# Kernel tuning notes

Measured on AMD Instinct MI355X. Metric: run time of the kernel, lower is better.

## Reference

```python
import jax, jax.numpy as jnp
import numpy as np

T, B, D, H = 512, 128, 256, 256
SIGMA = 0.01


def setup_inputs() -> dict:
    key = jax.random.key(0)
    ks = jax.random.split(key, 5)
    inputs = jax.random.normal(ks[0], (T, B, D), dtype=jnp.float32)
    W_xh_f = jax.random.normal(ks[1], (D, H), dtype=jnp.float32) * SIGMA
    W_hh_f = jax.random.normal(ks[2], (H, H), dtype=jnp.float32) * SIGMA
    b_h_f = jnp.zeros((H,), dtype=jnp.float32)
    W_xh_b = jax.random.normal(ks[3], (D, H), dtype=jnp.float32) * SIGMA
    W_hh_b = jax.random.normal(ks[4], (H, H), dtype=jnp.float32) * SIGMA
    b_h_b = jnp.zeros((H,), dtype=jnp.float32)
    return {"inputs": inputs, "W_xh_f": W_xh_f, "W_hh_f": W_hh_f, "b_h_f": b_h_f,
            "W_xh_b": W_xh_b, "W_hh_b": W_hh_b, "b_h_b": b_h_b}


def _rnn(inputs, W_xh, W_hh, b_h):
    # inputs: [T, B, D]; returns outputs [T, B, H], final state [B, H]
    h0 = jnp.zeros((inputs.shape[1], W_hh.shape[0]), dtype=inputs.dtype)
    # Precompute input projections for all steps (one big GEMM).
    xW = jnp.einsum('tbd,dh->tbh', inputs, W_xh) + b_h

    def step(h, xw_t):
        h = jnp.tanh(xw_t + h @ W_hh)
        return h, h

    hT, outs = jax.lax.scan(step, h0, xW)
    return outs, hT


def reference(inputs, W_xh_f, W_hh_f, b_h_f, W_xh_b, W_hh_b, b_h_b):
    f_outs, f_H = _rnn(inputs, W_xh_f, W_hh_f, b_h_f)          # forward direction
    b_outs, b_H = _rnn(inputs[::-1], W_xh_b, W_hh_b, b_h_b)    # backward direction
    # align backward outputs with original time order and concat on feature dim
    outputs = jnp.concatenate([f_outs, b_outs[::-1]], axis=-1)  # [T, B, 2H]
    return outputs, f_H, b_H
```

## Files before the change

kernel.cpp:

```cpp
#include <hip/hip_runtime.h>
#include <hip/hip_bf16.h>
#include <stdint.h>


typedef short sh8   __attribute__((ext_vector_type(8)));
typedef float f32x4 __attribute__((ext_vector_type(4)));

#define TT 512
#define BB 128
#define HH 256
#define LDH 264

__device__ __forceinline__ unsigned short f2bf(float x) {
    union { float f; unsigned u; } v; v.f = x;
    unsigned r = v.u + 0x7FFFu + ((v.u >> 16) & 1u);
    return (unsigned short)(r >> 16);
}
__device__ __forceinline__ unsigned pk2bf(float lo, float hi) {
    union { __hip_bfloat162 b; unsigned u; } c;
    c.b = __float22bfloat162_rn(make_float2(lo, hi));
    return c.u;
}
__device__ __forceinline__ float tanh5(float x) {
    float e = __builtin_amdgcn_exp2f(x * 2.8853900817779268f);
    return __builtin_fmaf(-2.0f, __builtin_amdgcn_rcpf(e + 1.0f), 1.0f);
}
__device__ __forceinline__ void bar_lds() {
    asm volatile("s_waitcnt lgkmcnt(0)\n\ts_barrier" ::: "memory");
}
__device__ __forceinline__ sh8 pack8(float4 a, float4 b) {
    union { sh8 s; unsigned u[4]; } c;
    c.u[0] = pk2bf(a.x, a.y); c.u[1] = pk2bf(a.z, a.w);
    c.u[2] = pk2bf(b.x, b.y); c.u[3] = pk2bf(b.z, b.w);
    return c.s;
}

__global__ __launch_bounds__(512, 2) void xw_precompute(
    const float* __restrict__ x,
    const float* __restrict__ Wxf, const float* __restrict__ bhf,
    const float* __restrict__ Wxb, const float* __restrict__ bhb,
    float* __restrict__ out)
{
    __shared__ __align__(16) unsigned short xb[2][16 * LDH];

    const int tid = threadIdx.x;
    const int w  = tid >> 6, l = tid & 63;
    const int li = l & 15, lq = l >> 4;
    const int N0 = w * 32;
    const int r0 = blockIdx.x * 256;

    sh8 wf[2][2][8];
#pragma unroll
    for (int d = 0; d < 2; ++d) {
        const float* W = d ? Wxb : Wxf;
#pragma unroll
        for (int nt = 0; nt < 2; ++nt)
#pragma unroll
            for (int kf = 0; kf < 8; ++kf) {
                sh8 t;
#pragma unroll
                for (int j = 0; j < 8; ++j)
                    t[j] = (short)f2bf(W[(size_t)(kf * 32 + lq * 8 + j) * HH + N0 + nt * 16 + li]);
                wf[d][nt][kf] = t;
            }
    }
    f32x4 bias4[2][2];
#pragma unroll
    for (int d = 0; d < 2; ++d) {
        const float* bs = d ? bhb : bhf;
#pragma unroll
        for (int nt = 0; nt < 2; ++nt)
            bias4[d][nt] = *(const f32x4*)&bs[N0 + nt * 16 + lq * 4];
    }

    const int sm = tid >> 5;
    const int sk = (tid & 31) * 8;
    const float* xrow = x + (size_t)(r0 + sm) * HH + sk;

    {
        float4 v0 = *(const float4*)xrow;
        float4 v1 = *(const float4*)(xrow + 4);
        *(sh8*)&xb[0][sm * LDH + sk] = pack8(v0, v1);
    }
    float4 xg0 = *(const float4*)(xrow + 16 * HH);
    float4 xg1 = *(const float4*)(xrow + 16 * HH + 4);
    bar_lds();

    float* obase = out + (size_t)(r0 + li) * 512 + N0 + lq * 4;

    for (int t = 0; t < 16; ++t) {
        const int cur = t & 1, nxt = cur ^ 1;
        {
            *(sh8*)&xb[nxt][sm * LDH + sk] = pack8(xg0, xg1);
            const int t2 = (t + 2 < 16) ? t + 2 : t;
            const float* p = xrow + (size_t)t2 * (16 * HH);
            xg0 = *(const float4*)p;
            xg1 = *(const float4*)(p + 4);
        }
        sh8 xf[8];
#pragma unroll
        for (int kf = 0; kf < 8; ++kf)
            xf[kf] = *(const sh8*)&xb[cur][li * LDH + kf * 32 + lq * 8];

        f32x4 acc[2][2];
#pragma unroll
        for (int d = 0; d < 2; ++d)
#pragma unroll
            for (int nt = 0; nt < 2; ++nt)
                acc[d][nt] = __builtin_amdgcn_mfma_f32_16x16x32_bf16(
                    wf[d][nt][0], xf[0], bias4[d][nt], 0, 0, 0);
#pragma unroll
        for (int kf = 1; kf < 8; ++kf)
#pragma unroll
            for (int d = 0; d < 2; ++d)
#pragma unroll
                for (int nt = 0; nt < 2; ++nt)
                    acc[d][nt] = __builtin_amdgcn_mfma_f32_16x16x32_bf16(
                        wf[d][nt][kf], xf[kf], acc[d][nt], 0, 0, 0);

        float* op = obase + (size_t)t * (16 * 512);
#pragma unroll
        for (int d = 0; d < 2; ++d)
#pragma unroll
            for (int nt = 0; nt < 2; ++nt)
                *(f32x4*)(op + d * HH + nt * 16) = acc[d][nt];
        bar_lds();
    }
}

__global__ __launch_bounds__(256, 1) void rnn_recur(
    const float* __restrict__ Whf, const float* __restrict__ Whb,
    float* __restrict__ out)
{
    __shared__ __align__(16) unsigned short hb[2][16 * LDH];

    const int tid = threadIdx.x;
    const int w  = tid >> 6, l = tid & 63;
    const int li = l & 15, lq = l >> 4;
    const int dir   = blockIdx.x >> 3;
    const int bbase = (blockIdx.x & 7) * 16;
    const float* Wh = dir ? Whb : Whf;
    const int N0 = w * 64;

    sh8 wfh[4][8];
#pragma unroll
    for (int nt = 0; nt < 4; ++nt)
#pragma unroll
        for (int kf = 0; kf < 8; ++kf) {
            sh8 t;
#pragma unroll
            for (int j = 0; j < 8; ++j)
                t[j] = (short)f2bf(Wh[(size_t)(kf * 32 + lq * 8 + j) * HH + N0 + nt * 16 + li]);
            wfh[nt][kf] = t;
        }

    for (int i = tid; i < 16 * LDH / 2; i += 256) ((unsigned*)hb[0])[i] = 0u;

    const ptrdiff_t ostep = dir ? -(ptrdiff_t)(BB * 512) : (ptrdiff_t)(BB * 512);
    const int t0 = dir ? TT - 1 : 0;
    float* op = out + (size_t)t0 * (BB * 512)
                    + (size_t)(bbase + li) * 512 + dir * HH + N0 + lq * 4;
    const float* pf = op + 2 * ostep;
    float* fsp = out + (size_t)TT * BB * 512 + (size_t)dir * (BB * HH)
                     + (size_t)(bbase + li) * HH + N0 + lq * 4;

    f32x4 xA[4], xB[4];
#pragma unroll
    for (int nt = 0; nt < 4; ++nt) {
        xA[nt] = *(const f32x4*)(op + nt * 16);
        xB[nt] = *(const f32x4*)(op + ostep + nt * 16);
    }

    const unsigned short* hr0 = &hb[0][li * LDH + lq * 8];
    const unsigned short* hr1 = &hb[1][li * LDH + lq * 8];
    unsigned short*       hw0 = &hb[0][li * LDH + N0 + lq * 4];
    unsigned short*       hw1 = &hb[1][li * LDH + N0 + lq * 4];

    bar_lds();

#define STEP(s_, HR, HW, XU)                                                    \
    do {                                                                        \
        sh8 hf[8];                                                              \
        _Pragma("unroll")                                                       \
        for (int kf = 0; kf < 8; ++kf)                                          \
            hf[kf] = *(const sh8*)(HR + kf * 32);                               \
        f32x4 acc[4];                                                           \
        _Pragma("unroll")                                                       \
        for (int nt = 0; nt < 4; ++nt)        \
            acc[nt] = __builtin_amdgcn_mfma_f32_16x16x32_bf16(                  \
                wfh[nt][0], hf[0], XU[nt], 0, 0, 0);                            \
        _Pragma("unroll")                                                       \
        for (int nt = 0; nt < 4; ++nt)              \
            XU[nt] = *(const f32x4*)(pf + nt * 16);                             \
        pf += ((s_) + 3 < TT) ? ostep : 0;           \
        _Pragma("unroll")                                                       \
        for (int kf = 1; kf < 8; ++kf)                                          \
            _Pragma("unroll")                                                   \
            for (int nt = 0; nt < 4; ++nt)                                      \
                acc[nt] = __builtin_amdgcn_mfma_f32_16x16x32_bf16(              \
                    wfh[nt][kf], hf[kf], acc[nt], 0, 0, 0);                     \
        f32x4 vv[4];                                                            \
        _Pragma("unroll")                                                       \
        for (int nt = 0; nt < 4; ++nt) {                                        \
            f32x4 v;                                                            \
            v[0] = tanh5(acc[nt][0]);                                           \
            v[1] = tanh5(acc[nt][1]);                                           \
            v[2] = tanh5(acc[nt][2]);                                           \
            v[3] = tanh5(acc[nt][3]);                                           \
            vv[nt] = v;                                                         \
            *(f32x4*)(op + nt * 16) = v;            \
            unsigned plo = pk2bf(v[0], v[1]);                                   \
            unsigned phi = pk2bf(v[2], v[3]);                                   \
            *(uint2*)(HW + nt * 16) = make_uint2(plo, phi);                     \
        }                                                                       \
        if ((s_) == TT - 1) {                                                   \
            _Pragma("unroll")                                                   \
            for (int nt = 0; nt < 4; ++nt)                                      \
                *(f32x4*)(fsp + nt * 16) = vv[nt];                              \
        }                                                                       \
        op += ostep;                                                            \
        bar_lds();                                                              \
    } while (0)

    for (int s = 0; s < TT; s += 2) {
        STEP(s,     hr0, hw1, xA);
        STEP(s + 1, hr1, hw0, xB);
    }
#undef STEP
}

extern "C" void kernel_launch(void* const* d_in, const int* in_sizes, int n_in,
                              void* d_out, int out_size, void* d_ws, size_t ws_size,
                              hipStream_t stream)
{
    const float* x   = (const float*)d_in[0];
    const float* Wxf = (const float*)d_in[1];
    const float* Whf = (const float*)d_in[2];
    const float* bhf = (const float*)d_in[3];
    const float* Wxb = (const float*)d_in[4];
    const float* Whb = (const float*)d_in[5];
    const float* bhb = (const float*)d_in[6];

    hipLaunchKernelGGL(xw_precompute, dim3(256), dim3(512), 0, stream,
                       x, Wxf, bhf, Wxb, bhb, (float*)d_out);
    hipLaunchKernelGGL(rnn_recur, dim3(16), dim3(256), 0, stream,
                       Whf, Whb, (float*)d_out);
}
```

Baseline: 689.7 us.

## Split precompute by direction and widen recurrence to 8 waves with deeper prefetch

The input-projection kernel now launches one block per direction and row chunk (512 blocks), so each block keeps half the weight fragments in registers. The recurrence kernel uses 512 threads (8 waves), each owning 32 output columns instead of 64. This halves the MFMA chain per wave on the serial critical path. It also deepens the xW prefetch to four steps and raises wave priority around the MFMA section. In exchange, every step's barrier now synchronises twice as many waves, and the x tile is loaded and converted twice in the precompute.

```diff
diff --git a/kernel.cpp b/kernel.cpp
--- a/kernel.cpp
+++ b/kernel.cpp
@@ -47,31 +47,26 @@
     const int w  = tid >> 6, l = tid & 63;
     const int li = l & 15, lq = l >> 4;
     const int N0 = w * 32;
-    const int r0 = blockIdx.x * 256;
-
-    sh8 wf[2][2][8];
-#pragma unroll
-    for (int d = 0; d < 2; ++d) {
-        const float* W = d ? Wxb : Wxf;
-#pragma unroll
-        for (int nt = 0; nt < 2; ++nt)
-#pragma unroll
-            for (int kf = 0; kf < 8; ++kf) {
-                sh8 t;
-#pragma unroll
-                for (int j = 0; j < 8; ++j)
-                    t[j] = (short)f2bf(W[(size_t)(kf * 32 + lq * 8 + j) * HH + N0 + nt * 16 + li]);
-                wf[d][nt][kf] = t;
-            }
-    }
-    f32x4 bias4[2][2];
-#pragma unroll
-    for (int d = 0; d < 2; ++d) {
-        const float* bs = d ? bhb : bhf;
-#pragma unroll
-        for (int nt = 0; nt < 2; ++nt)
-            bias4[d][nt] = *(const f32x4*)&bs[N0 + nt * 16 + lq * 4];
-    }
+    const int dir = blockIdx.x >> 8;
+    const int r0  = (blockIdx.x & 255) * 256;
+    const float* W  = dir ? Wxb : Wxf;
+    const float* bs = dir ? bhb : bhf;
+
+    sh8 wf[2][8];
+#pragma unroll
+    for (int nt = 0; nt < 2; ++nt)
+#pragma unroll
+        for (int kf = 0; kf < 8; ++kf) {
+            sh8 t;
+#pragma unroll
+            for (int j = 0; j < 8; ++j)
+                t[j] = (short)f2bf(W[(size_t)(kf * 32 + lq * 8 + j) * HH + N0 + nt * 16 + li]);
+            wf[nt][kf] = t;
+        }
+    f32x4 bias4[2];
+#pragma unroll
+    for (int nt = 0; nt < 2; ++nt)
+        bias4[nt] = *(const f32x4*)&bs[N0 + nt * 16 + lq * 4];
 
     const int sm = tid >> 5;
     const int sk = (tid & 31) * 8;
@@ -86,7 +81,7 @@
     float4 xg1 = *(const float4*)(xrow + 16 * HH + 4);
     bar_lds();
 
-    float* obase = out + (size_t)(r0 + li) * 512 + N0 + lq * 4;
+    float* obase = out + (size_t)(r0 + li) * 512 + dir * HH + N0 + lq * 4;
 
     for (int t = 0; t < 16; ++t) {
         const int cur = t & 1, nxt = cur ^ 1;
@@ -102,33 +97,27 @@
         for (int kf = 0; kf < 8; ++kf)
             xf[kf] = *(const sh8*)&xb[cur][li * LDH + kf * 32 + lq * 8];
 
-        f32x4 acc[2][2];
-#pragma unroll
-        for (int d = 0; d < 2; ++d)
+        f32x4 acc[2];
+#pragma unroll
+        for (int nt = 0; nt < 2; ++nt)
+            acc[nt] = __builtin_amdgcn_mfma_f32_16x16x32_bf16(
+                wf[nt][0], xf[0], bias4[nt], 0, 0, 0);
+#pragma unroll
+        for (int kf = 1; kf < 8; ++kf)
 #pragma unroll
             for (int nt = 0; nt < 2; ++nt)
-                acc[d][nt] = __builtin_amdgcn_mfma_f32_16x16x32_bf16(
-                    wf[d][nt][0], xf[0], bias4[d][nt], 0, 0, 0);
-#pragma unroll
-        for (int kf = 1; kf < 8; ++kf)
-#pragma unroll
-            for (int d = 0; d < 2; ++d)
-#pragma unroll
-                for (int nt = 0; nt < 2; ++nt)
-                    acc[d][nt] = __builtin_amdgcn_mfma_f32_16x16x32_bf16(
-                        wf[d][nt][kf], xf[kf], acc[d][nt], 0, 0, 0);
+                acc[nt] = __builtin_amdgcn_mfma_f32_16x16x32_bf16(
+                    wf[nt][kf], xf[kf], acc[nt], 0, 0, 0);
 
         float* op = obase + (size_t)t * (16 * 512);
 #pragma unroll
-        for (int d = 0; d < 2; ++d)
-#pragma unroll
-            for (int nt = 0; nt < 2; ++nt)
-                *(f32x4*)(op + d * HH + nt * 16) = acc[d][nt];
+        for (int nt = 0; nt < 2; ++nt)
+            *(f32x4*)(op + nt * 16) = acc[nt];
         bar_lds();
     }
 }
 
-__global__ __launch_bounds__(256, 1) void rnn_recur(
+__global__ __launch_bounds__(512, 2) void rnn_recur(
     const float* __restrict__ Whf, const float* __restrict__ Whb,
     float* __restrict__ out)
 {
@@ -140,11 +129,11 @@
     const int dir   = blockIdx.x >> 3;
     const int bbase = (blockIdx.x & 7) * 16;
     const float* Wh = dir ? Whb : Whf;
-    const int N0 = w * 64;
-
-    sh8 wfh[4][8];
-#pragma unroll
-    for (int nt = 0; nt < 4; ++nt)
+    const int N0 = w * 32;
+
+    sh8 wfh[2][8];
+#pragma unroll
+    for (int nt = 0; nt < 2; ++nt)
 #pragma unroll
         for (int kf = 0; kf < 8; ++kf) {
             sh8 t;
@@ -154,21 +143,23 @@
             wfh[nt][kf] = t;
         }
 
-    for (int i = tid; i < 16 * LDH / 2; i += 256) ((unsigned*)hb[0])[i] = 0u;
+    for (int i = tid; i < 16 * LDH / 2; i += 512) ((unsigned*)hb[0])[i] = 0u;
 
     const ptrdiff_t ostep = dir ? -(ptrdiff_t)(BB * 512) : (ptrdiff_t)(BB * 512);
     const int t0 = dir ? TT - 1 : 0;
     float* op = out + (size_t)t0 * (BB * 512)
                     + (size_t)(bbase + li) * 512 + dir * HH + N0 + lq * 4;
-    const float* pf = op + 2 * ostep;
+    const float* pf = op + 4 * ostep;
     float* fsp = out + (size_t)TT * BB * 512 + (size_t)dir * (BB * HH)
                      + (size_t)(bbase + li) * HH + N0 + lq * 4;
 
-    f32x4 xA[4], xB[4];
-#pragma unroll
-    for (int nt = 0; nt < 4; ++nt) {
-        xA[nt] = *(const f32x4*)(op + nt * 16);
-        xB[nt] = *(const f32x4*)(op + ostep + nt * 16);
+    f32x4 xA[2], xB[2], xC[2], xD[2];
+#pragma unroll
+    for (int nt = 0; nt < 2; ++nt) {
+        xA[nt] = *(const f32x4*)(op + 0 * ostep + nt * 16);
+        xB[nt] = *(const f32x4*)(op + 1 * ostep + nt * 16);
+        xC[nt] = *(const f32x4*)(op + 2 * ostep + nt * 16);
+        xD[nt] = *(const f32x4*)(op + 3 * ostep + nt * 16);
     }
 
     const unsigned short* hr0 = &hb[0][li * LDH + lq * 8];
@@ -184,24 +175,26 @@
         _Pragma("unroll")                                                       \
         for (int kf = 0; kf < 8; ++kf)                                          \
             hf[kf] = *(const sh8*)(HR + kf * 32);                               \
-        f32x4 acc[4];                                                           \
-        _Pragma("unroll")                                                       \
-        for (int nt = 0; nt < 4; ++nt)        \
+        f32x4 acc[2];                                                           \
+        __builtin_amdgcn_s_setprio(1);                                          \
+        _Pragma("unroll")                                                       \
+        for (int nt = 0; nt < 2; ++nt)        \
             acc[nt] = __builtin_amdgcn_mfma_f32_16x16x32_bf16(                  \
                 wfh[nt][0], hf[0], XU[nt], 0, 0, 0);                            \
         _Pragma("unroll")                                                       \
-        for (int nt = 0; nt < 4; ++nt)              \
+        for (int nt = 0; nt < 2; ++nt)              \
             XU[nt] = *(const f32x4*)(pf + nt * 16);                             \
-        pf += ((s_) + 3 < TT) ? ostep : 0;           \
+        pf += ((s_) + 5 < TT) ? ostep : 0;           \
         _Pragma("unroll")                                                       \
         for (int kf = 1; kf < 8; ++kf)                                          \
             _Pragma("unroll")                                                   \
-            for (int nt = 0; nt < 4; ++nt)                                      \
+            for (int nt = 0; nt < 2; ++nt)                                      \
                 acc[nt] = __builtin_amdgcn_mfma_f32_16x16x32_bf16(              \
                     wfh[nt][kf], hf[kf], acc[nt], 0, 0, 0);                     \
-        f32x4 vv[4];                                                            \
-        _Pragma("unroll")                                                       \
-        for (int nt = 0; nt < 4; ++nt) {                                        \
+        __builtin_amdgcn_s_setprio(0);                                          \
+        f32x4 vv[2];                                                            \
+        _Pragma("unroll")                                                       \
+        for (int nt = 0; nt < 2; ++nt) {                                        \
             f32x4 v;                                                            \
             v[0] = tanh5(acc[nt][0]);                                           \
             v[1] = tanh5(acc[nt][1]);                                           \
@@ -215,16 +208,18 @@
         }                                                                       \
         if ((s_) == TT - 1) {                                                   \
             _Pragma("unroll")                                                   \
-            for (int nt = 0; nt < 4; ++nt)                                      \
+            for (int nt = 0; nt < 2; ++nt)                                      \
                 *(f32x4*)(fsp + nt * 16) = vv[nt];                              \
         }                                                                       \
         op += ostep;                                                            \
         bar_lds();                                                              \
     } while (0)
 
-    for (int s = 0; s < TT; s += 2) {
+    for (int s = 0; s < TT; s += 4) {
         STEP(s,     hr0, hw1, xA);
         STEP(s + 1, hr1, hw0, xB);
+        STEP(s + 2, hr0, hw1, xC);
+        STEP(s + 3, hr1, hw0, xD);
     }
 #undef STEP
 }
@@ -241,8 +236,8 @@
     const float* Whb = (const float*)d_in[5];
     const float* bhb = (const float*)d_in[6];
 
-    hipLaunchKernelGGL(xw_precompute, dim3(256), dim3(512), 0, stream,
+    hipLaunchKernelGGL(xw_precompute, dim3(512), dim3(512), 0, stream,
                        x, Wxf, bhf, Wxb, bhb, (float*)d_out);
-    hipLaunchKernelGGL(rnn_recur, dim3(16), dim3(256), 0, stream,
+    hipLaunchKernelGGL(rnn_recur, dim3(16), dim3(512), 0, stream,
                        Whf, Whb, (float*)d_out);
 }
```

Result: faster. 635.7 us (-7.8%).

## Split recurrence across eight waves with dual MFMA accumulation chains

Applied to the files above, without the earlier changes.

Doubles the recurrence block to 512 threads so each wave owns 32 hidden columns instead of 64, which halves the serial per-step MFMA chain per wave. It splits the K reduction into two independent accumulator chains that are summed before tanh, prefetches the input projection four steps ahead, and raises wave priority around the MFMA section. The aim is to shorten the latency-bound critical path of each time step. In exchange, eight waves must now meet at every per-step barrier.

```diff
diff --git a/kernel.cpp b/kernel.cpp
--- a/kernel.cpp
+++ b/kernel.cpp
@@ -128,7 +128,7 @@
     }
 }
 
-__global__ __launch_bounds__(256, 1) void rnn_recur(
+__global__ __launch_bounds__(512, 2) void rnn_recur(
     const float* __restrict__ Whf, const float* __restrict__ Whb,
     float* __restrict__ out)
 {
@@ -140,11 +140,11 @@
     const int dir   = blockIdx.x >> 3;
     const int bbase = (blockIdx.x & 7) * 16;
     const float* Wh = dir ? Whb : Whf;
-    const int N0 = w * 64;
-
-    sh8 wfh[4][8];
-#pragma unroll
-    for (int nt = 0; nt < 4; ++nt)
+    const int N0 = w * 32;
+
+    sh8 wfh[2][8];
+#pragma unroll
+    for (int nt = 0; nt < 2; ++nt)
 #pragma unroll
         for (int kf = 0; kf < 8; ++kf) {
             sh8 t;
@@ -154,22 +154,25 @@
             wfh[nt][kf] = t;
         }
 
-    for (int i = tid; i < 16 * LDH / 2; i += 256) ((unsigned*)hb[0])[i] = 0u;
+    for (int i = tid; i < 16 * LDH / 2; i += 512) ((unsigned*)hb[0])[i] = 0u;
 
     const ptrdiff_t ostep = dir ? -(ptrdiff_t)(BB * 512) : (ptrdiff_t)(BB * 512);
     const int t0 = dir ? TT - 1 : 0;
     float* op = out + (size_t)t0 * (BB * 512)
                     + (size_t)(bbase + li) * 512 + dir * HH + N0 + lq * 4;
-    const float* pf = op + 2 * ostep;
+    const float* pf = op + 4 * ostep;
     float* fsp = out + (size_t)TT * BB * 512 + (size_t)dir * (BB * HH)
                      + (size_t)(bbase + li) * HH + N0 + lq * 4;
 
-    f32x4 xA[4], xB[4];
-#pragma unroll
-    for (int nt = 0; nt < 4; ++nt) {
-        xA[nt] = *(const f32x4*)(op + nt * 16);
-        xB[nt] = *(const f32x4*)(op + ostep + nt * 16);
-    }
+    f32x4 xA[2], xB[2], xC[2], xD[2];
+#pragma unroll
+    for (int nt = 0; nt < 2; ++nt) {
+        xA[nt] = *(const f32x4*)(op + 0 * ostep + nt * 16);
+        xB[nt] = *(const f32x4*)(op + 1 * ostep + nt * 16);
+        xC[nt] = *(const f32x4*)(op + 2 * ostep + nt * 16);
+        xD[nt] = *(const f32x4*)(op + 3 * ostep + nt * 16);
+    }
+    const f32x4 zero4 = (f32x4){0.f, 0.f, 0.f, 0.f};
 
     const unsigned short* hr0 = &hb[0][li * LDH + lq * 8];
     const unsigned short* hr1 = &hb[1][li * LDH + lq * 8];
@@ -184,29 +187,37 @@
         _Pragma("unroll")                                                       \
         for (int kf = 0; kf < 8; ++kf)                                          \
             hf[kf] = *(const sh8*)(HR + kf * 32);                               \
-        f32x4 acc[4];                                                           \
-        _Pragma("unroll")                                                       \
-        for (int nt = 0; nt < 4; ++nt)        \
+        f32x4 acc[2], acd[2];                                                   \
+        __builtin_amdgcn_s_setprio(1);                                          \
+        _Pragma("unroll")                                                       \
+        for (int nt = 0; nt < 2; ++nt) {         \
             acc[nt] = __builtin_amdgcn_mfma_f32_16x16x32_bf16(                  \
                 wfh[nt][0], hf[0], XU[nt], 0, 0, 0);                            \
-        _Pragma("unroll")                                                       \
-        for (int nt = 0; nt < 4; ++nt)              \
+            acd[nt] = __builtin_amdgcn_mfma_f32_16x16x32_bf16(                  \
+                wfh[nt][4], hf[4], zero4, 0, 0, 0);                             \
+        }                                                                       \
+        _Pragma("unroll")                                                       \
+        for (int nt = 0; nt < 2; ++nt)              \
             XU[nt] = *(const f32x4*)(pf + nt * 16);                             \
-        pf += ((s_) + 3 < TT) ? ostep : 0;           \
-        _Pragma("unroll")                                                       \
-        for (int kf = 1; kf < 8; ++kf)                                          \
+        pf += ((s_) + 5 < TT) ? ostep : 0;           \
+        _Pragma("unroll")                                                       \
+        for (int kf = 1; kf < 4; ++kf)                                          \
             _Pragma("unroll")                                                   \
-            for (int nt = 0; nt < 4; ++nt)                                      \
+            for (int nt = 0; nt < 2; ++nt) {                                    \
                 acc[nt] = __builtin_amdgcn_mfma_f32_16x16x32_bf16(              \
                     wfh[nt][kf], hf[kf], acc[nt], 0, 0, 0);                     \
-        f32x4 vv[4];                                                            \
-        _Pragma("unroll")                                                       \
-        for (int nt = 0; nt < 4; ++nt) {                                        \
+                acd[nt] = __builtin_amdgcn_mfma_f32_16x16x32_bf16(              \
+                    wfh[nt][kf + 4], hf[kf + 4], acd[nt], 0, 0, 0);             \
+            }                                                                   \
+        __builtin_amdgcn_s_setprio(0);                                          \
+        f32x4 vv[2];                                                            \
+        _Pragma("unroll")                                                       \
+        for (int nt = 0; nt < 2; ++nt) {                                        \
             f32x4 v;                                                            \
-            v[0] = tanh5(acc[nt][0]);                                           \
-            v[1] = tanh5(acc[nt][1]);                                           \
-            v[2] = tanh5(acc[nt][2]);                                           \
-            v[3] = tanh5(acc[nt][3]);                                           \
+            v[0] = tanh5(acc[nt][0] + acd[nt][0]);                              \
+            v[1] = tanh5(acc[nt][1] + acd[nt][1]);                              \
+            v[2] = tanh5(acc[nt][2] + acd[nt][2]);                              \
+            v[3] = tanh5(acc[nt][3] + acd[nt][3]);                              \
             vv[nt] = v;                                                         \
             *(f32x4*)(op + nt * 16) = v;            \
             unsigned plo = pk2bf(v[0], v[1]);                                   \
@@ -215,16 +226,18 @@
         }                                                                       \
         if ((s_) == TT - 1) {                                                   \
             _Pragma("unroll")                                                   \
-            for (int nt = 0; nt < 4; ++nt)                                      \
+            for (int nt = 0; nt < 2; ++nt)                                      \
                 *(f32x4*)(fsp + nt * 16) = vv[nt];                              \
         }                                                                       \
         op += ostep;                                                            \
         bar_lds();                                                              \
     } while (0)
 
-    for (int s = 0; s < TT; s += 2) {
+    for (int s = 0; s < TT; s += 4) {
         STEP(s,     hr0, hw1, xA);
         STEP(s + 1, hr1, hw0, xB);
+        STEP(s + 2, hr0, hw1, xC);
+        STEP(s + 3, hr1, hw0, xD);
     }
 #undef STEP
 }
@@ -243,6 +256,6 @@
 
     hipLaunchKernelGGL(xw_precompute, dim3(256), dim3(512), 0, stream,
                        x, Wxf, bhf, Wxb, bhb, (float*)d_out);
-    hipLaunchKernelGGL(rnn_recur, dim3(16), dim3(256), 0, stream,
+    hipLaunchKernelGGL(rnn_recur, dim3(16), dim3(512), 0, stream,
                        Whf, Whb, (float*)d_out);
 }
```

New measurement: 633.8 us. -8.1%, faster.
